# Kernel optimization log

Measured on AMD Instinct MI355X. Metric: run time of the kernel, lower is better.

The kernel has to match this reference:

```python
import jax, jax.numpy as jnp
import numpy as np

IN_DIM, OUT_DIM, N_BLOCKS, BLK_DIM = 256, 4, 2, 128
S, B = 1024, 128


def _u(key, shape, fan):
    lim = 1.0 / np.sqrt(fan)
    return jax.random.uniform(key, shape, jnp.float32, -lim, lim)


def _gru_params(key, i, h):
    k = jax.random.split(key, 4)
    return (_u(k[0], (3 * h, i), h), _u(k[1], (3 * h, h), h),
            _u(k[2], (3 * h,), h), _u(k[3], (3 * h,), h))


def gru_layer(x, wih, whh, bih, bhh):
    # x: (S, B, I) -> outputs (S, B, H); PyTorch GRU gate math, h0 = 0
    Bt = x.shape[1]
    H = whh.shape[1]
    xg = jnp.einsum('sbi,gi->sbg', x, wih) + bih  # (S, B, 3H) precomputed input gates

    def step(h, xg_t):
        hg = h @ whh.T + bhh
        xr, xz, xn = jnp.split(xg_t, 3, axis=-1)
        hr, hz, hn = jnp.split(hg, 3, axis=-1)
        r = jax.nn.sigmoid(xr + hr)
        z = jax.nn.sigmoid(xz + hz)
        n = jnp.tanh(xn + r * hn)
        h_new = (1.0 - z) * n + z * h
        return h_new, h_new

    h0 = jnp.zeros((Bt, H), x.dtype)
    _, ys = jax.lax.scan(step, h0, xg)
    return ys


def layernorm(x, g, b, eps=1e-5):
    m = jnp.mean(x, axis=-1, keepdims=True)
    v = jnp.mean(jnp.square(x - m), axis=-1, keepdims=True)
    return (x - m) * jax.lax.rsqrt(v + eps) * g + b


def setup_inputs() -> dict:
    key = jax.random.key(0)
    ks = jax.random.split(key, 16)
    d = {'x': jax.random.normal(ks[0], (S, B, IN_DIM), jnp.float32)}
    for nm, (i, h), kk in [('gru0', (IN_DIM, 2 * IN_DIM), ks[1]),
                           ('gru1', (IN_DIM // 2, IN_DIM), ks[2]),
                           ('gru2', (IN_DIM // 4, IN_DIM // 2), ks[3])]:
        wih, whh, bih, bhh = _gru_params(kk, i, h)
        d[nm + '_wih'], d[nm + '_whh'], d[nm + '_bih'], d[nm + '_bhh'] = wih, whh, bih, bhh
    d['d0_w'] = _u(ks[4], (BLK_DIM, 3 * 2 * IN_DIM), 3 * 2 * IN_DIM)
    d['d0_b'] = _u(ks[5], (BLK_DIM,), 3 * 2 * IN_DIM)
    for bi in range(N_BLOCKS):
        kb = jax.random.split(ks[6 + bi], 2)
        d[f'blk{bi}_ln_g'] = jnp.ones((BLK_DIM,), jnp.float32)
        d[f'blk{bi}_ln_b'] = jnp.zeros((BLK_DIM,), jnp.float32)
        wih, whh, bih, bhh = _gru_params(kb[0], BLK_DIM, BLK_DIM)
        d[f'blk{bi}_wih'], d[f'blk{bi}_whh'] = wih, whh
        d[f'blk{bi}_bih'], d[f'blk{bi}_bhh'] = bih, bhh
    d['df_w'] = _u(ks[10], (OUT_DIM, BLK_DIM), BLK_DIM)
    d['df_b'] = _u(ks[11], (OUT_DIM,), BLK_DIM)
    return d


def reference(x,
              gru0_wih, gru0_whh, gru0_bih, gru0_bhh,
              gru1_wih, gru1_whh, gru1_bih, gru1_bhh,
              gru2_wih, gru2_whh, gru2_bih, gru2_bhh,
              d0_w, d0_b,
              blk0_ln_g, blk0_ln_b, blk0_wih, blk0_whh, blk0_bih, blk0_bhh,
              blk1_ln_g, blk1_ln_b, blk1_wih, blk1_whh, blk1_bih, blk1_bhh,
              df_w, df_b):
    # branch 0: full-resolution features
    x0 = gru_layer(x, gru0_wih, gru0_whh, gru0_bih, gru0_bhh)            # (S,B,512)
    # branch 1: nearest-downsample features x0.5, GRU, nearest-upsample x2
    x1 = gru_layer(x[..., ::2], gru1_wih, gru1_whh, gru1_bih, gru1_bhh)  # (S,B,256)
    x1 = jnp.repeat(x1, 2, axis=-1)                                       # (S,B,512)
    # branch 2: nearest-downsample features x0.25, GRU, nearest-upsample x4
    x2 = gru_layer(x[..., ::4], gru2_wih, gru2_whh, gru2_bih, gru2_bhh)  # (S,B,128)
    x2 = jnp.repeat(x2, 4, axis=-1)                                       # (S,B,512)
    h = jnp.concatenate((x0, x1, x2), axis=-1)                            # (S,B,1536)
    h = jax.nn.relu(h @ d0_w.T + d0_b)                                    # (S,B,128)
    for (lg, lb, wih, whh, bih, bhh) in (
            (blk0_ln_g, blk0_ln_b, blk0_wih, blk0_whh, blk0_bih, blk0_bhh),
            (blk1_ln_g, blk1_ln_b, blk1_wih, blk1_whh, blk1_bih, blk1_bhh)):
        h = h + gru_layer(layernorm(h, lg, lb), wih, whh, bih, bhh)       # LN->GRU->residual
    return h @ df_w.T + df_b                                              # (S,B,4)
```

## Files before the change

kernel.cpp:

```cpp
#include <hip/hip_runtime.h>

typedef unsigned int u32;
typedef unsigned short u16;
typedef __attribute__((ext_vector_type(8))) short short8;
typedef __attribute__((ext_vector_type(4))) float f4;

#define MFMA16 __builtin_amdgcn_mfma_f32_16x16x32_bf16
#define ALOAD(p)    __hip_atomic_load((p), __ATOMIC_RELAXED, __HIP_MEMORY_SCOPE_AGENT)
#define ASTORE(p,v) __hip_atomic_store((p), (v), __ATOMIC_RELAXED, __HIP_MEMORY_SCOPE_AGENT)

#define OFF_XB    0LL
#define OFF_XD2   67108864LL
#define OFF_XD4   100663296LL
#define OFF_HCAT  117440512LL
#define OFF_LNB   352321536LL
#define OFF_H0R   385875968LL
#define OFF_Y0R   419430400LL
#define OFF_HB0   419561472LL
#define OFF_HB1   419823616LL
#define OFF_FLG   419954688LL
#define OFF_D0WF  420020224LL

__device__ __forceinline__ u16 f2bf(float f) {
  u32 u = __float_as_uint(f);
  return (u16)((u + 0x7fffu + ((u >> 16) & 1u)) >> 16);
}
__device__ __forceinline__ float bf2f(u32 b) { return __uint_as_float(b << 16); }
__device__ __forceinline__ float sigm(float x) { return __builtin_amdgcn_rcpf(1.f + __expf(-x)); }
__device__ __forceinline__ float tanh_(float x) { return 1.f - 2.f * __builtin_amdgcn_rcpf(1.f + __expf(2.f * x)); }

__device__ __forceinline__ short8 cvt8(const float* p) {
  short8 r;
#pragma unroll
  for (int j = 0; j < 8; ++j) r[j] = (short)f2bf(p[j]);
  return r;
}

template<int KH, int KX, int BT, int CSPAN, int WAVES, int GROUP_WGS, int PUB>
__device__ __forceinline__ void gru_scan(
    const float* __restrict__ wih, const float* __restrict__ whh,
    const float* __restrict__ bih, const float* __restrict__ bhh,
    const u16* __restrict__ xsrc,
    u16* __restrict__ outp, const int outPitch, const int outColBase,
    const int group, const int slab,
    u32* __restrict__ hbA, u32* __restrict__ hbB, u32* __restrict__ flags,
    char* sm)
{
  constexpr int H = KH;
  constexpr int KT = (KH + KX) / 32;
  constexpr int KH32 = KH / 32;
  constexpr int PITCH = (KH + KX) * 2 + 32;
  constexpr int CT_N = CSPAN / 16;
  constexpr int NTILES = (BT / 16) * CT_N;
  constexpr int MAXP = (NTILES + WAVES - 1) / WAVES;
  constexpr int NT = WAVES * 64;
  constexpr int NX = (BT * KX / 2) / NT;
  constexpr int NH = (BT * KH / 2) / NT;
  constexpr bool GH = (GROUP_WGS > 0);

  const int tid = threadIdx.x;
  const int l = tid & 63;
  const int wv = __builtin_amdgcn_readfirstlane(tid >> 6);
  const int lr = l & 15;
  const int lh = l >> 4;
  const long srow0 = group * BT;

  short8 Br[MAXP][KT], Bz[MAXP][KT], Bn[MAXP][KT];
  float bb0[MAXP], bb1[MAXP], bb2[MAXP], bb3[MAXP];
  float hk[MAXP][4];
#pragma unroll
  for (int p = 0; p < MAXP; ++p) {
    const int tp = wv + WAVES * p;
    const int tpc = (tp < NTILES) ? tp : 0;
    const int ct = tpc % CT_N;
    const int gcol = slab * CSPAN + ct * 16 + lr;
#pragma unroll
    for (int t = 0; t < KT; ++t) {
      const int k = t * 32 + lh * 8;
      if (t < KH32) {
        Br[p][t] = cvt8(whh + (long)(0 * H + gcol) * KH + k);
        Bz[p][t] = cvt8(whh + (long)(1 * H + gcol) * KH + k);
        Bn[p][t] = cvt8(whh + (long)(2 * H + gcol) * KH + k);
      } else {
        const int kx = k - KH;
        Br[p][t] = cvt8(wih + (long)(0 * H + gcol) * KX + kx);
        Bz[p][t] = cvt8(wih + (long)(1 * H + gcol) * KX + kx);
        Bn[p][t] = cvt8(wih + (long)(2 * H + gcol) * KX + kx);
      }
    }
    bb0[p] = bih[0 * H + gcol] + bhh[0 * H + gcol];
    bb1[p] = bih[1 * H + gcol] + bhh[1 * H + gcol];
    bb2[p] = bih[2 * H + gcol];
    bb3[p] = bhh[2 * H + gcol];
    hk[p][0] = hk[p][1] = hk[p][2] = hk[p][3] = 0.f;
  }

  if constexpr (!GH) {
#pragma unroll
    for (int i = 0; i < (BT * KH / 2 + NT - 1) / NT; ++i) {
      const int idx = tid + NT * i;
      if (idx < BT * KH / 2) {
        const int r = idx / (KH / 2), d = idx % (KH / 2);
        *(u32*)(sm + r * PITCH + ((d * 4) ^ ((r & 7) << 4))) = 0u;
      }
    }
  }

  u32 xr[NX];
#pragma unroll
  for (int i = 0; i < NX; ++i) {
    const int idx = tid + NT * i;
    const int r = idx / (KX / 2), d = idx % (KX / 2);
    xr[i] = *(const u32*)(xsrc + (srow0 + r) * KX + d * 2);
  }

  for (int s = 0; s < 1024; ++s) {
    if constexpr (GH) {
      if (wv == 0) {
        const u32 tgt = (u32)s;
        for (;;) {
          const u32 f = (l < GROUP_WGS) ? ALOAD(flags + l * 16) : tgt;
          if (__all(f >= tgt)) break;
        }
      }
      __syncthreads();
    }
#pragma unroll
    for (int i = 0; i < NX; ++i) {
      const int idx = tid + NT * i;
      const int r = idx / (KX / 2), d = idx % (KX / 2);
      *(u32*)(sm + r * PITCH + ((KH * 2 + d * 4) ^ ((r & 7) << 4))) = xr[i];
    }
    if constexpr (GH) {
      const u32* hb = (s & 1) ? hbB : hbA;
#pragma unroll
      for (int i = 0; i < NH; ++i) {
        const int idx = tid + NT * i;
        const int r = idx / (KH / 2), d = idx % (KH / 2);
        const u32 v = ALOAD(hb + r * (KH / 2) + d);
        *(u32*)(sm + r * PITCH + ((d * 4) ^ ((r & 7) << 4))) = v;
      }
    }
    if constexpr (!(GH || PUB)) {
      if (s + 1 < 1024) {
#pragma unroll
        for (int i = 0; i < NX; ++i) {
          const int idx = tid + NT * i;
          const int r = idx / (KX / 2), d = idx % (KX / 2);
          xr[i] = *(const u32*)(xsrc + ((s + 1) * 128L + srow0 + r) * KX + d * 2);
        }
      }
    }
    __syncthreads();

    u32 hnew[MAXP][4];
#pragma unroll
    for (int p = 0; p < MAXP; ++p) {
      const int tp = wv + WAVES * p;
      if (tp < NTILES) {
        const int mt = tp / CT_N;
        f4 ar = {0.f, 0.f, 0.f, 0.f}; f4 az = ar, anh = ar, anx = ar;
#pragma unroll
        for (int t = 0; t < KT; ++t) {
          const int row = mt * 16 + lr;
          const short8 a = *(const short8*)(sm + row * PITCH +
                              ((t * 64 + lh * 16) ^ ((row & 7) << 4)));
          ar = MFMA16(a, Br[p][t], ar, 0, 0, 0);
          az = MFMA16(a, Bz[p][t], az, 0, 0, 0);
          if (t < KH32) anh = MFMA16(a, Bn[p][t], anh, 0, 0, 0);
          else          anx = MFMA16(a, Bn[p][t], anx, 0, 0, 0);
        }
#pragma unroll
        for (int q = 0; q < 4; ++q) {
          const float rg = sigm(ar[q] + bb0[p]);
          const float zg = sigm(az[q] + bb1[p]);
          const float ng = tanh_(anx[q] + bb2[p] + rg * (anh[q] + bb3[p]));
          const float h = (1.f - zg) * ng + zg * hk[p][q];
          hk[p][q] = h;
          hnew[p][q] = f2bf(h);
        }
      }
    }
    if constexpr (!GH) __syncthreads();

#pragma unroll
    for (int p = 0; p < MAXP; ++p) {
      const int tp = wv + WAVES * p;
      if (tp < NTILES) {
        const int mt = tp / CT_N, ct = tp % CT_N;
        const int c = ct * 16 + lr;
#pragma unroll
        for (int q = 0; q < 4; ++q) {
          const u32 nb = (u32)__shfl_xor((int)hnew[p][q], 1);
          if ((l & 1) == 0) {
            const u32 pk = (hnew[p][q] & 0xffffu) | (nb << 16);
            const int b = mt * 16 + lh * 4 + q;
            u32* oa = (u32*)(outp + (s * 128L + srow0 + b) * outPitch + outColBase + c);
            if constexpr (GH) {
              u32* hbn = ((s + 1) & 1) ? hbB : hbA;
              ASTORE(hbn + b * (KH / 2) + (slab * CSPAN + c) / 2, pk);
              ASTORE(oa, pk);
            } else {
              *(u32*)(sm + b * PITCH + ((c * 2) ^ ((b & 7) << 4))) = pk;
              if constexpr (PUB) ASTORE(oa, pk); else *oa = pk;
            }
          }
        }
      }
    }
    if constexpr (GH || PUB) {
      __builtin_amdgcn_sched_barrier(0);
      if (s + 1 < 1024) {
#pragma unroll
        for (int i = 0; i < NX; ++i) {
          const int idx = tid + NT * i;
          const int r = idx / (KX / 2), d = idx % (KX / 2);
          xr[i] = ALOAD((const u32*)(xsrc + ((s + 1) * 128L + srow0 + r) * KX + d * 2));
        }
        __builtin_amdgcn_sched_barrier(0);
        asm volatile("s_waitcnt vmcnt(%0)" :: "i"(NX) : "memory");
      } else {
        asm volatile("s_waitcnt vmcnt(0)" ::: "memory");
      }
      __builtin_amdgcn_s_barrier();
      if (tid == 0) ASTORE(flags + (GH ? slab * 16 : 0), (u32)(s + 1));
    }
  }
}

__device__ __forceinline__ void gru0_scan(
    const float* __restrict__ wih, const float* __restrict__ whh,
    const float* __restrict__ bih, const float* __restrict__ bhh,
    const u16* __restrict__ x, u16* __restrict__ outp,
    const int group, const int slab,
    u32* __restrict__ hbA, u32* __restrict__ hbB, u32* __restrict__ flags,
    char* sm)
{
  constexpr int PITCH = 1568;
  const int tid = threadIdx.x;
  const int l = tid & 63;
  const int wv = __builtin_amdgcn_readfirstlane(tid >> 6);
  const int lr = l & 15, lh = l >> 4;
  const int ct = wv & 3, gg = wv >> 2;
  const long srow0 = group * 16;
  const int gcol = slab * 64 + ct * 16 + lr;
  f4* red = (f4*)(sm + 25088);

  short8 W0[24], W1[16];
#pragma unroll
  for (int t = 0; t < 24; ++t) {
    const int k = t * 32 + lh * 8;
    if (t < 16) W0[t] = cvt8(whh + (long)(gg * 512 + gcol) * 512 + k);
    else        W0[t] = cvt8(wih + (long)(gg * 512 + gcol) * 256 + (k - 512));
  }
  if (gg == 0) {
#pragma unroll
    for (int t = 0; t < 16; ++t)
      W1[t] = cvt8(whh + (long)(2 * 512 + gcol) * 512 + t * 32 + lh * 8);
  } else {
#pragma unroll
    for (int t = 0; t < 8; ++t)
      W1[t] = cvt8(wih + (long)(2 * 512 + gcol) * 256 + t * 32 + lh * 8);
  }
  const float bb0 = bih[0 * 512 + gcol] + bhh[0 * 512 + gcol];
  const float bb1 = bih[1 * 512 + gcol] + bhh[1 * 512 + gcol];
  const float bb2 = bih[2 * 512 + gcol];
  const float bb3 = bhh[2 * 512 + gcol];
  float hk[4] = {0.f, 0.f, 0.f, 0.f};

  u32 xr[4];
#pragma unroll
  for (int i = 0; i < 4; ++i) {
    const int idx = tid + 512 * i;
    const int r = idx >> 7, d = idx & 127;
    xr[i] = *(const u32*)(x + (srow0 + r) * 256 + d * 2);
  }

  for (int s = 0; s < 1024; ++s) {
    if (wv == 0) {
      const u32 tgt = (u32)s;
      for (;;) {
        const u32 f = (l < 8) ? ALOAD(flags + l * 16) : tgt;
        if (__all(f >= tgt)) break;
      }
    }
    __syncthreads();
#pragma unroll
    for (int i = 0; i < 4; ++i) {
      const int idx = tid + 512 * i;
      const int r = idx >> 7, d = idx & 127;
      *(u32*)(sm + r * PITCH + ((1024 + d * 4) ^ ((r & 7) << 4))) = xr[i];
    }
    {
      const u32* hb = (s & 1) ? hbB : hbA;
#pragma unroll
      for (int i = 0; i < 8; ++i) {
        const int idx = tid + 512 * i;
        const int r = idx >> 8, d = idx & 255;
        const u32 v = ALOAD(hb + r * 256 + d);
        *(u32*)(sm + r * PITCH + ((d * 4) ^ ((r & 7) << 4))) = v;
      }
    }
    __syncthreads();

    f4 a0 = {0.f, 0.f, 0.f, 0.f}, a1 = a0;
    if (gg == 0) {
#pragma unroll
      for (int t = 0; t < 24; ++t) {
        const short8 a = *(const short8*)(sm + lr * PITCH +
                            ((t * 64 + lh * 16) ^ ((lr & 7) << 4)));
        a0 = MFMA16(a, W0[t], a0, 0, 0, 0);
        if (t < 16) a1 = MFMA16(a, W1[t], a1, 0, 0, 0);
      }
    } else {
#pragma unroll
      for (int t = 0; t < 24; ++t) {
        const short8 a = *(const short8*)(sm + lr * PITCH +
                            ((t * 64 + lh * 16) ^ ((lr & 7) << 4)));
        a0 = MFMA16(a, W0[t], a0, 0, 0, 0);
        if (t >= 16) a1 = MFMA16(a, W1[t - 16], a1, 0, 0, 0);
      }
      red[(ct * 2 + 0) * 64 + l] = a0;
      red[(ct * 2 + 1) * 64 + l] = a1;
    }
    __syncthreads();
    if (gg == 0) {
      const f4 paz  = red[(ct * 2 + 0) * 64 + l];
      const f4 panx = red[(ct * 2 + 1) * 64 + l];
      u32 hnew[4];
#pragma unroll
      for (int q = 0; q < 4; ++q) {
        const float rg = sigm(a0[q] + bb0);
        const float zg = sigm(paz[q] + bb1);
        const float ng = tanh_(panx[q] + bb2 + rg * (a1[q] + bb3));
        const float h = (1.f - zg) * ng + zg * hk[q];
        hk[q] = h;
        hnew[q] = f2bf(h);
      }
      u32* hbn = ((s + 1) & 1) ? hbB : hbA;
#pragma unroll
      for (int q = 0; q < 4; ++q) {
        const u32 nb = (u32)__shfl_xor((int)hnew[q], 1);
        if ((l & 1) == 0) {
          const u32 pk = (hnew[q] & 0xffffu) | (nb << 16);
          const int b = lh * 4 + q;
          const int c = ct * 16 + lr;
          ASTORE(hbn + b * 256 + (slab * 64 + c) / 2, pk);
          ASTORE((u32*)(outp + (s * 128L + srow0 + b) * 896 + slab * 64 + c), pk);
        }
      }
    }
    __builtin_amdgcn_sched_barrier(0);
    if (s + 1 < 1024) {
#pragma unroll
      for (int i = 0; i < 4; ++i) {
        const int idx = tid + 512 * i;
        const int r = idx >> 7, d = idx & 127;
        xr[i] = ALOAD((const u32*)(x + ((s + 1) * 128L + srow0 + r) * 256 + d * 2));
      }
      __builtin_amdgcn_sched_barrier(0);
      asm volatile("s_waitcnt vmcnt(4)" ::: "memory");
    } else {
      asm volatile("s_waitcnt vmcnt(0)" ::: "memory");
    }
    __builtin_amdgcn_s_barrier();
    if (tid == 0) ASTORE(flags + slab * 16, (u32)(s + 1));
  }
}

struct MegaArgs {
  const float *w0ih, *w0hh, *b0ih, *b0hh;
  const float *w1ih, *w1hh, *b1ih, *b1hh;
  const float *w2ih, *w2hh, *b2ih, *b2hh;
  const u16 *xb, *xd2, *xd4;
  u16 *hcat, *lnb;
  u32 *h0r, *y0r, *hbuf0, *hbuf1, *flg;
  const u16 *d0wf; const float *d0b;
  const float *ln0g, *ln0b;
  const float *c0wih, *c0whh, *c0bih, *c0bhh;
  const float *ln1g, *ln1b;
  const float *c1wih, *c1whh, *c1bih, *c1bhh;
  const float *dfw, *dfb;
  float* out;
};

__device__ __forceinline__ void d0ln_scan(const MegaArgs& a, const int g,
                                          const int p, char* sm)
{
  const int tid = threadIdx.x;
  const int l = tid & 63;
  const int wv = __builtin_amdgcn_readfirstlane(tid >> 6);
  const int lr = l & 15, lh = l >> 4;
  const int dcol = wv * 16 + lr;
  u16* sA = (u16*)sm;
  float* part = (float*)(sm + 1536);
  float* rowstat = (float*)(sm + 3584);

  short8 Dw[28];
#pragma unroll
  for (int t = 0; t < 28; ++t)
    Dw[t] = *(const short8*)(a.d0wf + (long)dcol * 896 + t * 32 + lh * 8);
  const float dbias = a.d0b[dcol];
  const float lg = a.ln0g[dcol], lb = a.ln0b[dcol];

  const u32* hcat32 = (const u32*)a.hcat;
  u32* lnb32 = (u32*)a.lnb;
  const u32* pollp;
  if (l < 8)        pollp = a.flg + g * 128 + l * 16;
  else if (l < 16)  pollp = a.flg + 1024 + (g >> 1) * 128 + (l - 8) * 16;
  else if (l == 16) pollp = a.flg + 2048 + g * 16;
  else              pollp = a.flg + 12800 + g * 16;
  const int stg = (tid < 256);
  const int sr = tid >> 4, sc = tid & 15;

  for (int s = p; s < 1024; s += 8) {
    if (wv == 0) {
      const u32 tgt = (u32)(s + 1);
      for (;;) {
        u32 f = tgt;
        if (l < 17)       f = ALOAD(pollp);
        else if (l == 17) f = ALOAD(pollp) + 512;
        if (__all(f >= tgt)) break;
        __builtin_amdgcn_s_sleep(32);
      }
    }
    __syncthreads();
    const long rowbase = (long)s * 128 + g * 16;
    f4 acc = {0.f, 0.f, 0.f, 0.f};
    u32 vst = 0;
    if (stg) vst = ALOAD(hcat32 + (rowbase + sr) * 448 + sc);
    for (int kt = 0; kt < 28; ++kt) {
      u32 vnext = 0;
      if (kt + 1 < 28 && stg)
        vnext = ALOAD(hcat32 + (rowbase + sr) * 448 + (kt + 1) * 16 + sc);
      __syncthreads();
      if (stg) *(u32*)((char*)sA + sr * 80 + sc * 4) = vst;
      __syncthreads();
      const short8 af = *(const short8*)((char*)sA + lr * 80 + lh * 16);
      acc = MFMA16(af, Dw[kt], acc, 0, 0, 0);
      vst = vnext;
    }
    float v[4];
#pragma unroll
    for (int q = 0; q < 4; ++q) { const float xv = acc[q] + dbias; v[q] = xv > 0.f ? xv : 0.f; }
#pragma unroll
    for (int q = 0; q < 4; ++q) {
      float s1 = v[q], s2 = v[q] * v[q];
#pragma unroll
      for (int o = 1; o < 16; o <<= 1) { s1 += __shfl_xor(s1, o); s2 += __shfl_xor(s2, o); }
      if (lr == 0) {
        const int row = lh * 4 + q;
        part[(row * 8 + wv) * 2] = s1;
        part[(row * 8 + wv) * 2 + 1] = s2;
      }
    }
    __syncthreads();
    if (tid < 16) {
      float S1 = 0.f, S2 = 0.f;
#pragma unroll
      for (int w = 0; w < 8; ++w) { S1 += part[(tid * 8 + w) * 2]; S2 += part[(tid * 8 + w) * 2 + 1]; }
      const float m = S1 * 0.0078125f;
      const float rs = rsqrtf(S2 * 0.0078125f - m * m + 1e-5f);
      rowstat[tid * 2] = m; rowstat[tid * 2 + 1] = rs;
    }
    __syncthreads();
#pragma unroll
    for (int q = 0; q < 4; ++q) {
      const int row = lh * 4 + q;
      const float m = rowstat[row * 2], rs = rowstat[row * 2 + 1];
      const u16 lnq = f2bf((v[q] - m) * rs * lg + lb);
      const u32 nb = (u32)__shfl_xor((int)(u32)lnq, 1);
      if ((l & 1) == 0)
        ASTORE(lnb32 + (rowbase + row) * 64 + (dcol >> 1), ((u32)lnq & 0xffffu) | (nb << 16));
      ASTORE(a.h0r + ((long)(s & 511) * 128 + g * 16 + row) * 128 + dcol,
             __float_as_uint(v[q]));
    }
    asm volatile("s_waitcnt vmcnt(0)" ::: "memory");
    __syncthreads();
    if (tid == 0) ASTORE(a.flg + 4096 + g * 1024 + s, 1u);
  }
}

__device__ __forceinline__ void b0_scan(const MegaArgs& a, const int g, char* sm)
{
  const int tid = threadIdx.x, l = tid & 63;
  const int wv = __builtin_amdgcn_readfirstlane(tid >> 6);
  const int lr = l & 15, lh = l >> 4;
  const int gcol = wv * 16 + lr;
  char* T = sm;
  short8 Br[8], Bz[8], Bn[8];
#pragma unroll
  for (int t = 0; t < 8; ++t) {
    const int k = t * 32 + lh * 8;
    if (t < 4) {
      Br[t] = cvt8(a.c0whh + (long)(0 * 128 + gcol) * 128 + k);
      Bz[t] = cvt8(a.c0whh + (long)(1 * 128 + gcol) * 128 + k);
      Bn[t] = cvt8(a.c0whh + (long)(2 * 128 + gcol) * 128 + k);
    } else {
      const int kx = k - 128;
      Br[t] = cvt8(a.c0wih + (long)(0 * 128 + gcol) * 128 + kx);
      Bz[t] = cvt8(a.c0wih + (long)(1 * 128 + gcol) * 128 + kx);
      Bn[t] = cvt8(a.c0wih + (long)(2 * 128 + gcol) * 128 + kx);
    }
  }
  const float b0v = a.c0bih[gcol] + a.c0bhh[gcol];
  const float b1v = a.c0bih[128 + gcol] + a.c0bhh[128 + gcol];
  const float b2v = a.c0bih[256 + gcol];
  const float b3v = a.c0bhh[256 + gcol];
  float hk[4] = {0.f, 0.f, 0.f, 0.f};
#pragma unroll
  for (int i = 0; i < 2; ++i) {
    const int idx = tid + 512 * i; const int r = idx >> 6, d = idx & 63;
    *(u32*)(T + r * 544 + ((d * 4) ^ ((r & 7) << 4))) = 0u;
  }
  const u32* lnb32 = (const u32*)a.lnb;
  const u32* d0fp = a.flg + 4096 + g * 1024;
  const u32* ackp = a.flg + 12800 + g * 16;
  u32* myf = a.flg + 12544 + g * 16;
  __syncthreads();
  for (int s = 0; s < 1024; ++s) {
    if (wv == 0) {
      for (;;) {
        u32 f = 1u;
        if (l == 0)      f = ALOAD(d0fp + s);
        else if (l == 1) f = (ALOAD(ackp) + 3 >= (u32)s) ? 1u : 0u;
        if (__all(f >= 1u)) break;
        __builtin_amdgcn_s_sleep(4);
      }
    }
    __syncthreads();
#pragma unroll
    for (int i = 0; i < 2; ++i) {
      const int idx = tid + 512 * i; const int r = idx >> 6, d = idx & 63;
      const u32 xv = ALOAD(lnb32 + ((long)s * 128 + g * 16 + r) * 64 + d);
      *(u32*)(T + r * 544 + ((256 + d * 4) ^ ((r & 7) << 4))) = xv;
    }
    __syncthreads();
    f4 ar = {0.f, 0.f, 0.f, 0.f}; f4 az = ar, anh = ar, anx = ar;
#pragma unroll
    for (int t = 0; t < 8; ++t) {
      const short8 aa = *(const short8*)(T + lr * 544 + ((t * 64 + lh * 16) ^ ((lr & 7) << 4)));
      ar = MFMA16(aa, Br[t], ar, 0, 0, 0);
      az = MFMA16(aa, Bz[t], az, 0, 0, 0);
      if (t < 4) anh = MFMA16(aa, Bn[t], anh, 0, 0, 0);
      else       anx = MFMA16(aa, Bn[t], anx, 0, 0, 0);
    }
    u32 hnew[4];
#pragma unroll
    for (int q = 0; q < 4; ++q) {
      const float rg = sigm(ar[q] + b0v);
      const float zg = sigm(az[q] + b1v);
      const float ng = tanh_(anx[q] + b2v + rg * (anh[q] + b3v));
      const float h = (1.f - zg) * ng + zg * hk[q];
      hk[q] = h; hnew[q] = f2bf(h);
    }
    __syncthreads();
#pragma unroll
    for (int q = 0; q < 4; ++q) {
      const u32 nb = (u32)__shfl_xor((int)hnew[q], 1);
      if ((l & 1) == 0) {
        const u32 pk = (hnew[q] & 0xffffu) | (nb << 16);
        const int b = lh * 4 + q, c = wv * 16 + lr;
        *(u32*)(T + b * 544 + ((c * 2) ^ ((b & 7) << 4))) = pk;
        ASTORE(a.y0r + ((s & 3) * 8 + g) * 1024 + b * 64 + (c >> 1), pk);
      }
    }
    asm volatile("s_waitcnt vmcnt(0)" ::: "memory");
    __syncthreads();
    if (tid == 0) ASTORE(myf, (u32)(s + 1));
  }
}

__device__ __forceinline__ void b1_scan(const MegaArgs& a, const int g, char* sm)
{
  const int tid = threadIdx.x, l = tid & 63;
  const int wv = __builtin_amdgcn_readfirstlane(tid >> 6);
  const int lr = l & 15, lh = l >> 4;
  const int gcol = wv * 16 + lr;
  char* T = sm;
  float* SDF = (float*)(sm + 8704);
  float* SDB = (float*)(sm + 10752);
  short8 Br[8], Bz[8], Bn[8];
#pragma unroll
  for (int t = 0; t < 8; ++t) {
    const int k = t * 32 + lh * 8;
    if (t < 4) {
      Br[t] = cvt8(a.c1whh + (long)(0 * 128 + gcol) * 128 + k);
      Bz[t] = cvt8(a.c1whh + (long)(1 * 128 + gcol) * 128 + k);
      Bn[t] = cvt8(a.c1whh + (long)(2 * 128 + gcol) * 128 + k);
    } else {
      const int kx = k - 128;
      Br[t] = cvt8(a.c1wih + (long)(0 * 128 + gcol) * 128 + kx);
      Bz[t] = cvt8(a.c1wih + (long)(1 * 128 + gcol) * 128 + kx);
      Bn[t] = cvt8(a.c1wih + (long)(2 * 128 + gcol) * 128 + kx);
    }
  }
  const float b0v = a.c1bih[gcol] + a.c1bhh[gcol];
  const float b1v = a.c1bih[128 + gcol] + a.c1bhh[128 + gcol];
  const float b2v = a.c1bih[256 + gcol];
  const float b3v = a.c1bhh[256 + gcol];
  float hk[4] = {0.f, 0.f, 0.f, 0.f};
#pragma unroll
  for (int i = 0; i < 2; ++i) {
    const int idx = tid + 512 * i; const int r = idx >> 6, d = idx & 63;
    *(u32*)(T + r * 544 + ((d * 4) ^ ((r & 7) << 4))) = 0u;
  }
  SDF[tid] = a.dfw[tid];
  if (tid < 4) SDB[tid] = a.dfb[tid];
  const int rr = tid >> 5, cq = tid & 31, c4 = cq * 4;
  const float g1a = a.ln1g[c4], g1b = a.ln1g[c4 + 1], g1c = a.ln1g[c4 + 2], g1d = a.ln1g[c4 + 3];
  const float h1a = a.ln1b[c4], h1b = a.ln1b[c4 + 1], h1c = a.ln1b[c4 + 2], h1d = a.ln1b[c4 + 3];
  const u32* y0fp = a.flg + 12544 + g * 16;
  u32* ackp = a.flg + 12800 + g * 16;
  __syncthreads();
  for (int s = 0; s < 1024; ++s) {
    if (wv == 0) {
      const u32 tgt = (u32)(s + 1);
      for (;;) {
        const u32 f = (l == 0) ? ALOAD(y0fp) : tgt;
        if (__all(f >= tgt)) break;
        __builtin_amdgcn_s_sleep(4);
      }
    }
    __syncthreads();
    const u32 ya = ALOAD(a.y0r + ((s & 3) * 8 + g) * 1024 + rr * 64 + cq * 2);
    const u32 yb = ALOAD(a.y0r + ((s & 3) * 8 + g) * 1024 + rr * 64 + cq * 2 + 1);
    const long hbase = ((long)(s & 511) * 128 + g * 16 + rr) * 128 + c4;
    const float p0 = __uint_as_float(ALOAD(a.h0r + hbase));
    const float p1 = __uint_as_float(ALOAD(a.h0r + hbase + 1));
    const float p2 = __uint_as_float(ALOAD(a.h0r + hbase + 2));
    const float p3 = __uint_as_float(ALOAD(a.h0r + hbase + 3));
    const float u0 = p0 + bf2f(ya & 0xffffu);
    const float u1 = p1 + bf2f(ya >> 16);
    const float u2 = p2 + bf2f(yb & 0xffffu);
    const float u3 = p3 + bf2f(yb >> 16);
    float s1 = u0 + u1 + u2 + u3;
    float s2 = u0 * u0 + u1 * u1 + u2 * u2 + u3 * u3;
#pragma unroll
    for (int o = 1; o < 32; o <<= 1) { s1 += __shfl_xor(s1, o); s2 += __shfl_xor(s2, o); }
    const float m = s1 * 0.0078125f;
    const float rs = rsqrtf(s2 * 0.0078125f - m * m + 1e-5f);
    const u32 q0 = (u32)f2bf((u0 - m) * rs * g1a + h1a) |
                   ((u32)f2bf((u1 - m) * rs * g1b + h1b) << 16);
    const u32 q1 = (u32)f2bf((u2 - m) * rs * g1c + h1c) |
                   ((u32)f2bf((u3 - m) * rs * g1d + h1d) << 16);
    char* xa = T + rr * 544 + ((256 + cq * 8) ^ ((rr & 7) << 4));
    *(u32*)xa = q0;
    *(u32*)(xa + 4) = q1;
    __syncthreads();
    if (tid == 0) ASTORE(ackp, (u32)(s + 1));
    f4 ar = {0.f, 0.f, 0.f, 0.f}; f4 az = ar, anh = ar, anx = ar;
#pragma unroll
    for (int t = 0; t < 8; ++t) {
      const short8 aa = *(const short8*)(T + lr * 544 + ((t * 64 + lh * 16) ^ ((lr & 7) << 4)));
      ar = MFMA16(aa, Br[t], ar, 0, 0, 0);
      az = MFMA16(aa, Bz[t], az, 0, 0, 0);
      if (t < 4) anh = MFMA16(aa, Bn[t], anh, 0, 0, 0);
      else       anx = MFMA16(aa, Bn[t], anx, 0, 0, 0);
    }
    u32 hnew[4];
#pragma unroll
    for (int q = 0; q < 4; ++q) {
      const float rg = sigm(ar[q] + b0v);
      const float zg = sigm(az[q] + b1v);
      const float ng = tanh_(anx[q] + b2v + rg * (anh[q] + b3v));
      const float h = (1.f - zg) * ng + zg * hk[q];
      hk[q] = h; hnew[q] = f2bf(h);
    }
    __syncthreads();
#pragma unroll
    for (int q = 0; q < 4; ++q) {
      const u32 nb = (u32)__shfl_xor((int)hnew[q], 1);
      if ((l & 1) == 0) {
        const u32 pk = (hnew[q] & 0xffffu) | (nb << 16);
        const int b = lh * 4 + q, c = wv * 16 + lr;
        *(u32*)(T + b * 544 + ((c * 2) ^ ((b & 7) << 4))) = pk;
      }
    }
    __syncthreads();
    const int yo = (c4 * 2) ^ ((rr & 7) << 4);
    const u32 za = *(const u32*)(T + rr * 544 + yo);
    const u32 zb = *(const u32*)(T + rr * 544 + yo + 4);
    const float w0 = u0 + bf2f(za & 0xffffu);
    const float w1 = u1 + bf2f(za >> 16);
    const float w2 = u2 + bf2f(zb & 0xffffu);
    const float w3 = u3 + bf2f(zb >> 16);
    float pp0 = w0 * SDF[c4]       + w1 * SDF[c4 + 1]       + w2 * SDF[c4 + 2]       + w3 * SDF[c4 + 3];
    float pp1 = w0 * SDF[128 + c4] + w1 * SDF[128 + c4 + 1] + w2 * SDF[128 + c4 + 2] + w3 * SDF[128 + c4 + 3];
    float pp2 = w0 * SDF[256 + c4] + w1 * SDF[256 + c4 + 1] + w2 * SDF[256 + c4 + 2] + w3 * SDF[256 + c4 + 3];
    float pp3 = w0 * SDF[384 + c4] + w1 * SDF[384 + c4 + 1] + w2 * SDF[384 + c4 + 2] + w3 * SDF[384 + c4 + 3];
#pragma unroll
    for (int o = 1; o < 32; o <<= 1) {
      pp0 += __shfl_xor(pp0, o); pp1 += __shfl_xor(pp1, o);
      pp2 += __shfl_xor(pp2, o); pp3 += __shfl_xor(pp3, o);
    }
    if (cq == 0) {
      f4 ov = {pp0 + SDB[0], pp1 + SDB[1], pp2 + SDB[2], pp3 + SDB[3]};
      *(f4*)(a.out + ((long)s * 128 + g * 16 + rr) * 4) = ov;
    }
  }
}

__global__ void __launch_bounds__(512, 2) mega(MegaArgs a) {
  __shared__ __align__(16) char sm[33280];
  const int bid = blockIdx.x;
  if (bid < 64) {
    const int group = bid & 7, slab = bid >> 3;
    gru0_scan(a.w0ih, a.w0hh, a.b0ih, a.b0hh, a.xb, a.hcat, group, slab,
              a.hbuf0 + group * 4096, a.hbuf0 + 32768 + group * 4096,
              a.flg + group * 128, sm);
  } else if (bid < 96) {
    const int id = bid - 64, G = id & 3, slab = id >> 2;
    gru_scan<256, 128, 32, 32, 8, 8, 0>(a.w1ih, a.w1hh, a.b1ih, a.b1hh, a.xd2,
        a.hcat, 896, 512 + slab * 32, G, slab,
        a.hbuf1 + G * 4096, a.hbuf1 + 16384 + G * 4096,
        a.flg + 1024 + G * 128, sm);
  } else if (bid < 104) {
    const int g = bid - 96;
    gru_scan<128, 64, 16, 128, 8, 0, 1>(a.w2ih, a.w2hh, a.b2ih, a.b2hh, a.xd4,
        a.hcat, 896, 768, g, 0, nullptr, nullptr,
        a.flg + 2048 + g * 16, sm);
  } else if (bid < 168) {
    const int id = bid - 104;
    d0ln_scan(a, id & 7, id >> 3, sm);
  } else if (bid < 176) {
    b0_scan(a, bid - 168, sm);
  } else {
    b1_scan(a, bid - 176, sm);
  }
}

__global__ void __launch_bounds__(256) prep(const float* __restrict__ x,
    u16* __restrict__ xb, u16* __restrict__ xd2, u16* __restrict__ xd4,
    const float* __restrict__ d0w, u16* __restrict__ d0wf) {
  const int b = blockIdx.x;
  if (b < 16384) {
    const long t = b * 256L + threadIdx.x;
    const f4 aa = ((const f4*)x)[t * 2];
    const f4 cc = ((const f4*)x)[t * 2 + 1];
    const u16 u0 = f2bf(aa[0]), u1 = f2bf(aa[1]), u2 = f2bf(aa[2]), u3 = f2bf(aa[3]);
    const u16 u4 = f2bf(cc[0]), u5 = f2bf(cc[1]), u6 = f2bf(cc[2]), u7 = f2bf(cc[3]);
    short8 s8; s8[0]=(short)u0; s8[1]=(short)u1; s8[2]=(short)u2; s8[3]=(short)u3;
    s8[4]=(short)u4; s8[5]=(short)u5; s8[6]=(short)u6; s8[7]=(short)u7;
    *(short8*)(xb + t * 8) = s8;
    const long row = t >> 5; const int ch = (int)(t & 31);
    *(u32*)(xd2 + row * 128 + ch * 4)     = (u32)u0 | ((u32)u2 << 16);
    *(u32*)(xd2 + row * 128 + ch * 4 + 2) = (u32)u4 | ((u32)u6 << 16);
    *(u32*)(xd4 + row * 64 + ch * 2)      = (u32)u0 | ((u32)u4 << 16);
  } else {
    const int idx = (b - 16384) * 256 + threadIdx.x;
    const int o = idx / 896, c = idx % 896;
    float v;
    if (c < 512) v = d0w[o * 1536 + c];
    else if (c < 768) { const int j = c - 512; v = d0w[o * 1536 + 512 + 2 * j] + d0w[o * 1536 + 513 + 2 * j]; }
    else { const int j = c - 768; const float* p = d0w + o * 1536 + 1024 + 4 * j; v = p[0] + p[1] + p[2] + p[3]; }
    d0wf[idx] = f2bf(v);
  }
}

extern "C" void kernel_launch(void* const* d_in, const int* in_sizes, int n_in,
                              void* d_out, int out_size, void* d_ws, size_t ws_size,
                              hipStream_t stream) {
  char* ws = (char*)d_ws;
  const float* x     = (const float*)d_in[0];
  const float* g0wih = (const float*)d_in[1];
  const float* g0whh = (const float*)d_in[2];
  const float* g0bih = (const float*)d_in[3];
  const float* g0bhh = (const float*)d_in[4];
  const float* g1wih = (const float*)d_in[5];
  const float* g1whh = (const float*)d_in[6];
  const float* g1bih = (const float*)d_in[7];
  const float* g1bhh = (const float*)d_in[8];
  const float* g2wih = (const float*)d_in[9];
  const float* g2whh = (const float*)d_in[10];
  const float* g2bih = (const float*)d_in[11];
  const float* g2bhh = (const float*)d_in[12];
  const float* d0w   = (const float*)d_in[13];
  const float* d0b   = (const float*)d_in[14];
  const float* ln0g  = (const float*)d_in[15];
  const float* ln0b  = (const float*)d_in[16];
  const float* b0wih = (const float*)d_in[17];
  const float* b0whh = (const float*)d_in[18];
  const float* b0bih = (const float*)d_in[19];
  const float* b0bhh = (const float*)d_in[20];
  const float* ln1g  = (const float*)d_in[21];
  const float* ln1b  = (const float*)d_in[22];
  const float* b1wih = (const float*)d_in[23];
  const float* b1whh = (const float*)d_in[24];
  const float* b1bih = (const float*)d_in[25];
  const float* b1bhh = (const float*)d_in[26];
  const float* dfw   = (const float*)d_in[27];
  const float* dfb   = (const float*)d_in[28];

  MegaArgs a;
  a.w0ih = g0wih; a.w0hh = g0whh; a.b0ih = g0bih; a.b0hh = g0bhh;
  a.w1ih = g1wih; a.w1hh = g1whh; a.b1ih = g1bih; a.b1hh = g1bhh;
  a.w2ih = g2wih; a.w2hh = g2whh; a.b2ih = g2bih; a.b2hh = g2bhh;
  a.xb  = (u16*)(ws + OFF_XB);
  a.xd2 = (u16*)(ws + OFF_XD2);
  a.xd4 = (u16*)(ws + OFF_XD4);
  a.hcat = (u16*)(ws + OFF_HCAT);
  a.lnb  = (u16*)(ws + OFF_LNB);
  a.h0r  = (u32*)(ws + OFF_H0R);
  a.y0r  = (u32*)(ws + OFF_Y0R);
  a.hbuf0 = (u32*)(ws + OFF_HB0);
  a.hbuf1 = (u32*)(ws + OFF_HB1);
  a.flg   = (u32*)(ws + OFF_FLG);
  a.d0wf  = (u16*)(ws + OFF_D0WF);
  a.d0b = d0b; a.ln0g = ln0g; a.ln0b = ln0b;
  a.c0wih = b0wih; a.c0whh = b0whh; a.c0bih = b0bih; a.c0bhh = b0bhh;
  a.ln1g = ln1g; a.ln1b = ln1b;
  a.c1wih = b1wih; a.c1whh = b1whh; a.c1bih = b1bih; a.c1bhh = b1bhh;
  a.dfw = dfw; a.dfb = dfb;
  a.out = (float*)d_out;

  hipMemsetAsync(ws + OFF_HB0, 0, (size_t)(OFF_D0WF - OFF_HB0), stream);

  prep<<<16832, 256, 0, stream>>>(x, (u16*)(ws + OFF_XB), (u16*)(ws + OFF_XD2),
                                  (u16*)(ws + OFF_XD4), d0w, (u16*)(ws + OFF_D0WF));

  mega<<<184, 512, 0, stream>>>(a);
}
```

Before: 4.952 ms.

## Defer output stores past flag publish and relax consumer polling to step+2

The GRU scan kernels now issue the recurrent hidden-state stores first and the sequence-output stores afterwards. The vmcnt wait before publishing the step flag counts the output stores as still in flight, so only the hidden-state exchange is on the critical path. The __syncthreads after polling becomes a bare s_barrier. Because outputs may land one step late, the downstream dense consumer now waits for flag s+2 from the gru0/gru1 producers, which adds some consumer lag and a subtle memory-ordering dependency.

```diff
diff --git a/kernel.cpp b/kernel.cpp
--- a/kernel.cpp
+++ b/kernel.cpp
@@ -123,7 +123,7 @@
           if (__all(f >= tgt)) break;
         }
       }
-      __syncthreads();
+      __builtin_amdgcn_s_barrier();
     }
 #pragma unroll
     for (int i = 0; i < NX; ++i) {
@@ -183,6 +183,7 @@
     }
     if constexpr (!GH) __syncthreads();
 
+    u32 pkv[MAXP][4];
 #pragma unroll
     for (int p = 0; p < MAXP; ++p) {
       const int tp = wv + WAVES * p;
@@ -192,23 +193,37 @@
 #pragma unroll
         for (int q = 0; q < 4; ++q) {
           const u32 nb = (u32)__shfl_xor((int)hnew[p][q], 1);
+          pkv[p][q] = (hnew[p][q] & 0xffffu) | (nb << 16);
           if ((l & 1) == 0) {
-            const u32 pk = (hnew[p][q] & 0xffffu) | (nb << 16);
+            const int b = mt * 16 + lh * 4 + q;
+            if constexpr (GH) {
+              u32* hbn = ((s + 1) & 1) ? hbB : hbA;
+              ASTORE(hbn + b * (KH / 2) + (slab * CSPAN + c) / 2, pkv[p][q]);
+            } else {
+              *(u32*)(sm + b * PITCH + ((c * 2) ^ ((b & 7) << 4))) = pkv[p][q];
+            }
+          }
+        }
+      }
+    }
+    __builtin_amdgcn_sched_barrier(0);
+#pragma unroll
+    for (int p = 0; p < MAXP; ++p) {
+      const int tp = wv + WAVES * p;
+      if (tp < NTILES) {
+        const int mt = tp / CT_N, ct = tp % CT_N;
+        const int c = ct * 16 + lr;
+#pragma unroll
+        for (int q = 0; q < 4; ++q) {
+          if ((l & 1) == 0) {
             const int b = mt * 16 + lh * 4 + q;
             u32* oa = (u32*)(outp + (s * 128L + srow0 + b) * outPitch + outColBase + c);
-            if constexpr (GH) {
-              u32* hbn = ((s + 1) & 1) ? hbB : hbA;
-              ASTORE(hbn + b * (KH / 2) + (slab * CSPAN + c) / 2, pk);
-              ASTORE(oa, pk);
-            } else {
-              *(u32*)(sm + b * PITCH + ((c * 2) ^ ((b & 7) << 4))) = pk;
-              if constexpr (PUB) ASTORE(oa, pk); else *oa = pk;
-            }
+            if constexpr (GH || PUB) ASTORE(oa, pkv[p][q]); else *oa = pkv[p][q];
           }
         }
       }
     }
-    if constexpr (GH || PUB) {
+    if constexpr (GH) {
       __builtin_amdgcn_sched_barrier(0);
       if (s + 1 < 1024) {
 #pragma unroll
@@ -218,12 +233,28 @@
           xr[i] = ALOAD((const u32*)(xsrc + ((s + 1) * 128L + srow0 + r) * KX + d * 2));
         }
         __builtin_amdgcn_sched_barrier(0);
+        asm volatile("s_waitcnt vmcnt(%0)" :: "i"(MAXP * 4 + NX) : "memory");
+      } else {
+        asm volatile("s_waitcnt vmcnt(0)" ::: "memory");
+      }
+      __builtin_amdgcn_s_barrier();
+      if (tid == 0) ASTORE(flags + slab * 16, (u32)(s + 1));
+    } else if constexpr (PUB) {
+      __builtin_amdgcn_sched_barrier(0);
+      if (s + 1 < 1024) {
+#pragma unroll
+        for (int i = 0; i < NX; ++i) {
+          const int idx = tid + NT * i;
+          const int r = idx / (KX / 2), d = idx % (KX / 2);
+          xr[i] = ALOAD((const u32*)(xsrc + ((s + 1) * 128L + srow0 + r) * KX + d * 2));
+        }
+        __builtin_amdgcn_sched_barrier(0);
         asm volatile("s_waitcnt vmcnt(%0)" :: "i"(NX) : "memory");
       } else {
         asm volatile("s_waitcnt vmcnt(0)" ::: "memory");
       }
       __builtin_amdgcn_s_barrier();
-      if (tid == 0) ASTORE(flags + (GH ? slab * 16 : 0), (u32)(s + 1));
+      if (tid == 0) ASTORE(flags, (u32)(s + 1));
     }
   }
 }
@@ -284,7 +315,7 @@
         if (__all(f >= tgt)) break;
       }
     }
-    __syncthreads();
+    __builtin_amdgcn_s_barrier();
 #pragma unroll
     for (int i = 0; i < 4; ++i) {
       const int idx = tid + 512 * i;
@@ -324,6 +355,7 @@
       red[(ct * 2 + 1) * 64 + l] = a1;
     }
     __syncthreads();
+    u32 pkv[4];
     if (gg == 0) {
       const f4 paz  = red[(ct * 2 + 0) * 64 + l];
       const f4 panx = red[(ct * 2 + 1) * 64 + l];
@@ -341,12 +373,20 @@
 #pragma unroll
       for (int q = 0; q < 4; ++q) {
         const u32 nb = (u32)__shfl_xor((int)hnew[q], 1);
+        pkv[q] = (hnew[q] & 0xffffu) | (nb << 16);
         if ((l & 1) == 0) {
-          const u32 pk = (hnew[q] & 0xffffu) | (nb << 16);
           const int b = lh * 4 + q;
           const int c = ct * 16 + lr;
-          ASTORE(hbn + b * 256 + (slab * 64 + c) / 2, pk);
-          ASTORE((u32*)(outp + (s * 128L + srow0 + b) * 896 + slab * 64 + c), pk);
+          ASTORE(hbn + b * 256 + (slab * 64 + c) / 2, pkv[q]);
+        }
+      }
+      __builtin_amdgcn_sched_barrier(0);
+#pragma unroll
+      for (int q = 0; q < 4; ++q) {
+        if ((l & 1) == 0) {
+          const int b = lh * 4 + q;
+          const int c = ct * 16 + lr;
+          ASTORE((u32*)(outp + (s * 128L + srow0 + b) * 896 + slab * 64 + c), pkv[q]);
         }
       }
     }
@@ -359,7 +399,7 @@
         xr[i] = ALOAD((const u32*)(x + ((s + 1) * 128L + srow0 + r) * 256 + d * 2));
       }
       __builtin_amdgcn_sched_barrier(0);
-      asm volatile("s_waitcnt vmcnt(4)" ::: "memory");
+      asm volatile("s_waitcnt vmcnt(8)" ::: "memory");
     } else {
       asm volatile("s_waitcnt vmcnt(0)" ::: "memory");
     }
@@ -415,12 +455,14 @@
 
   for (int s = p; s < 1024; s += 8) {
     if (wv == 0) {
-      const u32 tgt = (u32)(s + 1);
+      const u32 t01 = (u32)((s + 2 < 1024) ? s + 2 : 1024);
+      const u32 t2  = (u32)(s + 1);
       for (;;) {
-        u32 f = tgt;
-        if (l < 17)       f = ALOAD(pollp);
-        else if (l == 17) f = ALOAD(pollp) + 512;
-        if (__all(f >= tgt)) break;
+        int ok = 1;
+        if (l < 16)       ok = (ALOAD(pollp) >= t01);
+        else if (l == 16) ok = (ALOAD(pollp) >= t2);
+        else if (l == 17) ok = (ALOAD(pollp) + 512 >= t2);
+        if (__all(ok)) break;
         __builtin_amdgcn_s_sleep(32);
       }
     }
```

New measurement: 4.568 ms. -7.8%, faster.
